# Kernel optimization log

Measured on AMD Instinct MI355X. Metric: run time of the kernel, lower is better.

The kernel has to match this reference:

```python
import jax, jax.numpy as jnp
import numpy as np
import math

B, S, D = 4, 2048, 1024
H, HD = 16, 64
RANK = 16
SCALING = 32.0 / RANK  # alpha / rank = 2.0


def setup_inputs() -> dict:
    key = jax.random.key(0)
    ks = jax.random.split(key, 12)
    s = 1.0 / math.sqrt(D)
    inp = {
        "hidden_states": jax.random.normal(ks[0], (B, S, D), dtype=jnp.float32),
        "attention_mask": jnp.zeros((B, 1, 1, S), dtype=jnp.float32),
        "Wq": jax.random.normal(ks[1], (D, D), dtype=jnp.float32) * s,
        "bq": jnp.zeros((D,), dtype=jnp.float32),
        "Aq": jax.random.normal(ks[2], (RANK, D), dtype=jnp.float32) * s,
        "Bq": jax.random.normal(ks[3], (D, RANK), dtype=jnp.float32) * 0.02,
        "Wk": jax.random.normal(ks[4], (D, D), dtype=jnp.float32) * s,
        "bk": jnp.zeros((D,), dtype=jnp.float32),
        "Wv": jax.random.normal(ks[5], (D, D), dtype=jnp.float32) * s,
        "bv": jnp.zeros((D,), dtype=jnp.float32),
        "Av": jax.random.normal(ks[6], (RANK, D), dtype=jnp.float32) * s,
        "Bv": jax.random.normal(ks[7], (D, RANK), dtype=jnp.float32) * 0.02,
        "Wo": jax.random.normal(ks[8], (D, D), dtype=jnp.float32) * s,
        "bo": jnp.zeros((D,), dtype=jnp.float32),
    }
    return inp


def _lora_linear(x, W, b, A, Bm):
    # F.linear(x, W, b) + (x @ A.T @ B.T) * scaling
    return x @ W.T + b + ((x @ A.T) @ Bm.T) * SCALING


def reference(hidden_states, attention_mask, Wq, bq, Aq, Bq, Wk, bk, Wv, bv, Av, Bv, Wo, bo):
    x = hidden_states
    q = _lora_linear(x, Wq, bq, Aq, Bq)          # [B,S,D]
    k = x @ Wk.T + bk                             # [B,S,D]
    v = _lora_linear(x, Wv, bv, Av, Bv)           # [B,S,D]

    def split_heads(t):
        return t.reshape(B, S, H, HD).transpose(0, 2, 1, 3)  # [B,H,S,HD]

    q, k, v = split_heads(q), split_heads(k), split_heads(v)
    scores = jnp.einsum("bhqd,bhkd->bhqk", q, k) / math.sqrt(HD)  # [B,H,S,S]
    scores = scores + attention_mask
    attn = jax.nn.softmax(scores, axis=-1)
    ctx = jnp.einsum("bhqk,bhkd->bhqd", attn, v)  # [B,H,S,HD]
    ctx = ctx.transpose(0, 2, 1, 3).reshape(B, S, D)
    return ctx @ Wo.T + bo
```

## Files before the change

### kernel.cpp

```cpp
#include <hip/hip_runtime.h>
#include <cstdint>


#define D_DIM 1024
#define S_DIM 2048
#define B_DIM 4
#define H_DIM 16
#define HD_DIM 64
#define M_DIM 8192
#define LOG2E 1.44269504f

typedef __bf16 bf16;
typedef unsigned int u32;
typedef __bf16 bf16x2v __attribute__((ext_vector_type(2)));
typedef __bf16 bf16x4v __attribute__((ext_vector_type(4)));
typedef __bf16 bf16x8 __attribute__((ext_vector_type(8)));
typedef float f32x4 __attribute__((ext_vector_type(4)));

typedef __attribute__((address_space(1))) void* as1p;
typedef __attribute__((address_space(3))) void* as3p;

__device__ __forceinline__ void gll16(const void* g, void* l) {
  __builtin_amdgcn_global_load_lds((as1p)(g), (as3p)(l), 16, 0, 0);
}

__device__ __forceinline__ u32 pack_bf16(float lo, float hi) {
  bf16x2v t;
  t[0] = (bf16)lo;
  t[1] = (bf16)hi;
  return __builtin_bit_cast(u32, t);
}

__global__ void convert_x_kernel(const float* __restrict__ x, bf16* __restrict__ xb) {
  const int i = (blockIdx.x * 256 + threadIdx.x) * 8;
  const float4 a = *(const float4*)(x + i);
  const float4 b = *(const float4*)(x + i + 4);
  bf16x8 o;
  o[0] = (bf16)a.x; o[1] = (bf16)a.y; o[2] = (bf16)a.z; o[3] = (bf16)a.w;
  o[4] = (bf16)b.x; o[5] = (bf16)b.y; o[6] = (bf16)b.z; o[7] = (bf16)b.w;
  *(bf16x8*)(xb + i) = o;
}

__global__ void prep_w_kernel(const float* __restrict__ W, const float* __restrict__ A,
                              const float* __restrict__ Bm, bf16* __restrict__ out,
                              int use_lora) {
  const int i = blockIdx.x * 256 + threadIdx.x;
  const int n = i >> 10, k = i & (D_DIM - 1);
  float w = W[i];
  if (use_lora) {
    float acc = 0.f;
#pragma unroll
    for (int r = 0; r < 16; ++r) acc = fmaf(Bm[n * 16 + r], A[r * D_DIM + k], acc);
    w += 2.0f * acc;
  }
  out[i] = (bf16)w;
}

__global__ __launch_bounds__(256) void gemm_qkv_kernel(
    const bf16* __restrict__ X, const bf16* __restrict__ Wqkv,
    const float* __restrict__ bq, const float* __restrict__ bk,
    const float* __restrict__ bv, bf16* __restrict__ Qo, bf16* __restrict__ Ko,
    bf16* __restrict__ Vo) {
  __shared__ __attribute__((aligned(16))) bf16 As[2][128 * 64];
  __shared__ __attribute__((aligned(16))) bf16 Bs[2][128 * 64];
  const int tid = threadIdx.x;
  const int wave = tid >> 6, lane = tid & 63;
  const int quad = lane >> 4, l16 = lane & 15;
  const int m0 = blockIdx.x * 128, n0 = blockIdx.y * 128;
  const int wm = (wave >> 1) * 64, wn = (wave & 1) * 64;
  const int srow = lane >> 3, sblk = lane & 7;

  const f32x4 zero = {0.f, 0.f, 0.f, 0.f};
  f32x4 acc[4][4];
#pragma unroll
  for (int mi = 0; mi < 4; ++mi)
#pragma unroll
    for (int ni = 0; ni < 4; ++ni) acc[mi][ni] = zero;

  auto stage = [&](int kt) {
    const int buf = kt & 1, kb = kt * 64;
#pragma unroll
    for (int it = 0; it < 4; ++it) {
      const int c = it * 4 + wave;
      const int row = c * 8 + srow;
      const int b = sblk ^ (row & 7);
      gll16(X + (size_t)(m0 + row) * D_DIM + kb + b * 8, &As[buf][c * 512 + lane * 8]);
      gll16(Wqkv + (size_t)(n0 + row) * D_DIM + kb + b * 8, &Bs[buf][c * 512 + lane * 8]);
    }
  };
  stage(0);

  for (int kt = 0; kt < D_DIM / 64; ++kt) {
    __syncthreads();
    if (kt + 1 < D_DIM / 64) stage(kt + 1);
    const bf16* as_ = &As[kt & 1][0];
    const bf16* bs_ = &Bs[kt & 1][0];
#pragma unroll
    for (int ks = 0; ks < 2; ++ks) {
      bf16x8 af[4], bfr[4];
#pragma unroll
      for (int mi = 0; mi < 4; ++mi) {
        const int row = wm + mi * 16 + l16;
        af[mi] = *(const bf16x8*)(as_ + row * 64 + (((ks * 4 + quad) ^ (row & 7)) * 8));
      }
#pragma unroll
      for (int ni = 0; ni < 4; ++ni) {
        const int row = wn + ni * 16 + l16;
        bfr[ni] = *(const bf16x8*)(bs_ + row * 64 + (((ks * 4 + quad) ^ (row & 7)) * 8));
      }
#pragma unroll
      for (int mi = 0; mi < 4; ++mi)
#pragma unroll
        for (int ni = 0; ni < 4; ++ni)
          acc[mi][ni] =
              __builtin_amdgcn_mfma_f32_16x16x32_bf16(af[mi], bfr[ni], acc[mi][ni], 0, 0, 0);
    }
  }

  const int sel = n0 >> 10;
  const float* bp = (sel == 0) ? bq : (sel == 1) ? bk : bv;
  const float qs = 0.125f * LOG2E;

  if (sel == 2) {
#pragma unroll
    for (int ni = 0; ni < 4; ++ni) {
      const int c = (n0 + wn + ni * 16 + l16) & 1023;
      const int h = c >> 6, hd = c & 63;
      const float bvv = bp[c];
#pragma unroll
      for (int mi = 0; mi < 4; ++mi) {
        const int row0 = m0 + wm + mi * 16 + quad * 4;
        const int b = row0 >> 11, s0 = row0 & (S_DIM - 1);
        bf16x4v pk;
#pragma unroll
        for (int r = 0; r < 4; ++r) pk[r] = (bf16)(acc[mi][ni][r] + bvv);
        *(bf16x4v*)(Vo + ((size_t)(b * H_DIM + h) * HD_DIM + hd) * S_DIM + s0) = pk;
      }
    }
  } else {
    bf16* O = (sel == 0) ? Qo : Ko;
#pragma unroll
    for (int ni = 0; ni < 4; ++ni) {
      const int c = (n0 + wn + ni * 16 + l16) & 1023;
      const int h = c >> 6, hd = c & 63;
      const float bvv = bp[c];
#pragma unroll
      for (int mi = 0; mi < 4; ++mi) {
#pragma unroll
        for (int r = 0; r < 4; ++r) {
          const int row = m0 + wm + mi * 16 + quad * 4 + r;
          const int b = row >> 11, s = row & (S_DIM - 1);
          float v = acc[mi][ni][r] + bvv;
          if (sel == 0) v *= qs;
          O[((size_t)(b * H_DIM + h) * S_DIM + s) * HD_DIM + hd] = (bf16)v;
        }
      }
    }
  }
}

__global__ __launch_bounds__(256) void gemm_o_kernel(const bf16* __restrict__ X,
                                                     const bf16* __restrict__ W,
                                                     const float* __restrict__ bias,
                                                     float* __restrict__ out) {
  __shared__ __attribute__((aligned(16))) bf16 As[2][128 * 64];
  __shared__ __attribute__((aligned(16))) bf16 Bs[2][128 * 64];
  const int tid = threadIdx.x;
  const int wave = tid >> 6, lane = tid & 63;
  const int quad = lane >> 4, l16 = lane & 15;
  const int m0 = blockIdx.x * 128, n0 = blockIdx.y * 128;
  const int wm = (wave >> 1) * 64, wn = (wave & 1) * 64;
  const int srow = lane >> 3, sblk = lane & 7;

  const f32x4 zero = {0.f, 0.f, 0.f, 0.f};
  f32x4 acc[4][4];
#pragma unroll
  for (int mi = 0; mi < 4; ++mi)
#pragma unroll
    for (int ni = 0; ni < 4; ++ni) acc[mi][ni] = zero;

  auto stage = [&](int kt) {
    const int buf = kt & 1, kb = kt * 64;
#pragma unroll
    for (int it = 0; it < 4; ++it) {
      const int c = it * 4 + wave;
      const int row = c * 8 + srow;
      const int b = sblk ^ (row & 7);
      gll16(X + (size_t)(m0 + row) * D_DIM + kb + b * 8, &As[buf][c * 512 + lane * 8]);
      gll16(W + (size_t)(n0 + row) * D_DIM + kb + b * 8, &Bs[buf][c * 512 + lane * 8]);
    }
  };
  stage(0);

  for (int kt = 0; kt < D_DIM / 64; ++kt) {
    __syncthreads();
    if (kt + 1 < D_DIM / 64) stage(kt + 1);
    const bf16* as_ = &As[kt & 1][0];
    const bf16* bs_ = &Bs[kt & 1][0];
#pragma unroll
    for (int ks = 0; ks < 2; ++ks) {
      bf16x8 af[4], bfr[4];
#pragma unroll
      for (int mi = 0; mi < 4; ++mi) {
        const int row = wm + mi * 16 + l16;
        af[mi] = *(const bf16x8*)(as_ + row * 64 + (((ks * 4 + quad) ^ (row & 7)) * 8));
      }
#pragma unroll
      for (int ni = 0; ni < 4; ++ni) {
        const int row = wn + ni * 16 + l16;
        bfr[ni] = *(const bf16x8*)(bs_ + row * 64 + (((ks * 4 + quad) ^ (row & 7)) * 8));
      }
#pragma unroll
      for (int mi = 0; mi < 4; ++mi)
#pragma unroll
        for (int ni = 0; ni < 4; ++ni)
          acc[mi][ni] =
              __builtin_amdgcn_mfma_f32_16x16x32_bf16(af[mi], bfr[ni], acc[mi][ni], 0, 0, 0);
    }
  }
#pragma unroll
  for (int ni = 0; ni < 4; ++ni) {
    const int col = n0 + wn + ni * 16 + l16;
    const float bv = bias[col];
#pragma unroll
    for (int mi = 0; mi < 4; ++mi)
#pragma unroll
      for (int r = 0; r < 4; ++r) {
        const int row = m0 + wm + mi * 16 + quad * 4 + r;
        out[(size_t)row * D_DIM + col] = acc[mi][ni][r] + bv;
      }
  }
}

__global__ __launch_bounds__(512, 4) void attn_kernel(const bf16* __restrict__ Q,
                                                      const bf16* __restrict__ K,
                                                      const bf16* __restrict__ Vt,
                                                      const float* __restrict__ mask,
                                                      bf16* __restrict__ ctx) {
  __shared__ __attribute__((aligned(16))) bf16 Ks[2][64 * 64];
  __shared__ __attribute__((aligned(16))) bf16 Vs[2][64 * 64];
  __shared__ __attribute__((aligned(16))) float cms[S_DIM];

  const int tid = threadIdx.x;
  const int wave = tid >> 6, lane = tid & 63;
  const int quad = lane >> 4, l16 = lane & 15;
  const int bh = blockIdx.y, b = bh >> 4, h = bh & 15;
  const int qt = blockIdx.x;

  const bf16* Qg = Q + ((size_t)bh * S_DIM + qt * 256 + wave * 32) * HD_DIM;
  bf16x8 qf[2][2];
#pragma unroll
  for (int nq = 0; nq < 2; ++nq)
#pragma unroll
    for (int ks = 0; ks < 2; ++ks)
      qf[nq][ks] = *(const bf16x8*)(Qg + (nq * 16 + l16) * HD_DIM + ks * 32 + quad * 8);

  {
    const float* mp = mask + b * S_DIM + tid * 4;
    const float4 a = *(const float4*)(mp);
    f32x4 r0 = {fmaf(a.x, LOG2E, -16.f), fmaf(a.y, LOG2E, -16.f),
                fmaf(a.z, LOG2E, -16.f), fmaf(a.w, LOG2E, -16.f)};
    *(f32x4*)(cms + tid * 4) = r0;
  }

  bf16x8 onef;
#pragma unroll
  for (int j = 0; j < 8; ++j) onef[j] = (bf16)1.0f;

  const f32x4 zero = {0.f, 0.f, 0.f, 0.f};
  f32x4 o[2][4], osum[2];
#pragma unroll
  for (int nq = 0; nq < 2; ++nq) {
    osum[nq] = zero;
#pragma unroll
    for (int nh = 0; nh < 4; ++nh) o[nq][nh] = zero;
  }

  const bf16* Kg0 = K + (size_t)bh * S_DIM * HD_DIM;
  const bf16* Vg0 = Vt + (size_t)bh * HD_DIM * S_DIM;

  auto stage = [&](int t) {
    const int buf = t & 1;
    const bf16* Kg = Kg0 + (size_t)t * 64 * HD_DIM;
    const bf16* Vg = Vg0 + t * 64;
    const int c = wave;
    const int row = c * 8 + (lane >> 3);
    const int blk = (lane & 7) ^ (row & 7);
    gll16(Kg + (size_t)row * HD_DIM + blk * 8, &Ks[buf][c * 512 + lane * 8]);
    gll16(Vg + (size_t)row * S_DIM + blk * 8, &Vs[buf][c * 512 + lane * 8]);
  };
  stage(0);

  for (int t = 0; t < S_DIM / 64; ++t) {
    __syncthreads();
    if (t + 1 < S_DIM / 64) stage(t + 1);
    const bf16* ks_ = &Ks[t & 1][0];
    const bf16* vs_ = &Vs[t & 1][0];

#pragma unroll
    for (int half = 0; half < 2; ++half) {
      u32 pk[2][2][2];
#pragma unroll
      for (int mtl = 0; mtl < 2; ++mtl) {
        const int mt = half * 2 + mtl;
        const f32x4 cm = *(const f32x4*)(cms + t * 64 + mt * 16 + quad * 4);
        f32x4 sc[2];
        sc[0] = cm;
        sc[1] = cm;
#pragma unroll
        for (int ks = 0; ks < 2; ++ks) {
          const int row = mt * 16 + l16;
          const bf16x8 kf =
              *(const bf16x8*)(ks_ + row * 64 + (((ks * 4 + quad) ^ (row & 7)) * 8));
#pragma unroll
          for (int nq = 0; nq < 2; ++nq)
            sc[nq] = __builtin_amdgcn_mfma_f32_16x16x32_bf16(kf, qf[nq][ks], sc[nq], 0, 0, 0);
        }
#pragma unroll
        for (int nq = 0; nq < 2; ++nq) {
          const float e0 = __builtin_amdgcn_exp2f(sc[nq][0]);
          const float e1 = __builtin_amdgcn_exp2f(sc[nq][1]);
          const float e2 = __builtin_amdgcn_exp2f(sc[nq][2]);
          const float e3 = __builtin_amdgcn_exp2f(sc[nq][3]);
          pk[nq][mtl][0] = pack_bf16(e0, e1);
          pk[nq][mtl][1] = pack_bf16(e2, e3);
        }
      }

      bf16x8 vf[4];
#pragma unroll
      for (int nh = 0; nh < 4; ++nh) {
        const int vrow = nh * 16 + l16;
        vf[nh] = *(const bf16x8*)(vs_ + vrow * 64 + (((half * 4 + quad) ^ (vrow & 7)) * 8));
      }

#pragma unroll
      for (int nq = 0; nq < 2; ++nq) {
        auto a0 = __builtin_amdgcn_permlane32_swap(pk[nq][0][0], pk[nq][1][0], false, false);
        auto a1 = __builtin_amdgcn_permlane32_swap(pk[nq][0][1], pk[nq][1][1], false, false);
        auto b0 = __builtin_amdgcn_permlane16_swap(a0[0], a0[1], false, false);
        auto b1 = __builtin_amdgcn_permlane16_swap(a1[0], a1[1], false, false);
        union {
          u32 w[4];
          bf16x8 v;
        } pu;
        pu.w[0] = b0[0];
        pu.w[1] = b1[0];
        pu.w[2] = b0[1];
        pu.w[3] = b1[1];
        const bf16x8 pf = pu.v;
#pragma unroll
        for (int nh = 0; nh < 4; ++nh)
          o[nq][nh] = __builtin_amdgcn_mfma_f32_16x16x32_bf16(pf, vf[nh], o[nq][nh], 0, 0, 0);
        osum[nq] = __builtin_amdgcn_mfma_f32_16x16x32_bf16(pf, onef, osum[nq], 0, 0, 0);
      }
    }
  }

#pragma unroll
  for (int nq = 0; nq < 2; ++nq)
#pragma unroll
    for (int r = 0; r < 4; ++r) {
      const float inv = 1.0f / osum[nq][r];
      const int s = qt * 256 + wave * 32 + nq * 16 + quad * 4 + r;
#pragma unroll
      for (int nh = 0; nh < 4; ++nh)
        ctx[((size_t)b * S_DIM + s) * D_DIM + h * 64 + nh * 16 + l16] =
            (bf16)(o[nq][nh][r] * inv);
    }
}

extern "C" void kernel_launch(void* const* d_in, const int* in_sizes, int n_in,
                              void* d_out, int out_size, void* d_ws, size_t ws_size,
                              hipStream_t stream) {
  const float* x    = (const float*)d_in[0];
  const float* mask = (const float*)d_in[1];
  const float* Wq   = (const float*)d_in[2];
  const float* bq   = (const float*)d_in[3];
  const float* Aq   = (const float*)d_in[4];
  const float* Bq   = (const float*)d_in[5];
  const float* Wk   = (const float*)d_in[6];
  const float* bk   = (const float*)d_in[7];
  const float* Wv   = (const float*)d_in[8];
  const float* bv   = (const float*)d_in[9];
  const float* Av   = (const float*)d_in[10];
  const float* Bv   = (const float*)d_in[11];
  const float* Wo   = (const float*)d_in[12];
  const float* bo   = (const float*)d_in[13];
  float* out = (float*)d_out;

  bf16* xb   = (bf16*)d_ws;
  bf16* wqkv = xb + (size_t)M_DIM * D_DIM;
  bf16* wo   = wqkv + (size_t)3 * D_DIM * D_DIM;
  bf16* Qw   = wo + (size_t)D_DIM * D_DIM;
  bf16* Kw   = Qw + (size_t)M_DIM * D_DIM;
  bf16* Vw   = Kw + (size_t)M_DIM * D_DIM;
  bf16* Cw   = xb;

  convert_x_kernel<<<M_DIM * D_DIM / (256 * 8), 256, 0, stream>>>(x, xb);
  prep_w_kernel<<<D_DIM * D_DIM / 256, 256, 0, stream>>>(Wq, Aq, Bq, wqkv, 1);
  prep_w_kernel<<<D_DIM * D_DIM / 256, 256, 0, stream>>>(Wk, nullptr, nullptr,
                                                         wqkv + (size_t)D_DIM * D_DIM, 0);
  prep_w_kernel<<<D_DIM * D_DIM / 256, 256, 0, stream>>>(Wv, Av, Bv,
                                                         wqkv + (size_t)2 * D_DIM * D_DIM, 1);
  prep_w_kernel<<<D_DIM * D_DIM / 256, 256, 0, stream>>>(Wo, nullptr, nullptr, wo, 0);

  gemm_qkv_kernel<<<dim3(M_DIM / 128, 3 * D_DIM / 128), 256, 0, stream>>>(
      xb, wqkv, bq, bk, bv, Qw, Kw, Vw);

  attn_kernel<<<dim3(S_DIM / 256, B_DIM * H_DIM), 512, 0, stream>>>(Qw, Kw, Vw, mask, Cw);

  gemm_o_kernel<<<dim3(M_DIM / 128, D_DIM / 128), 256, 0, stream>>>(Cw, wo, bo, out);
}
```

Baseline: 293.1 us.

## Rewrite QKV GEMM as 256x256 tile with 8-wave ping-pong pipelined schedule

The QKV projection GEMM moves from 128x128 tiles with 4 waves to 256x256 tiles with 8 waves. Each wave now computes a 128x64 sub-tile. The K loop is restructured into a hand-scheduled ping-pong: LDS fragment reads, async global-to-LDS staging of A/B halves, and MFMA bursts are interleaved with explicit barriers, vmcnt waits, and setprio around the MFMA blocks. The aim is more data reuse per tile and overlap of memory traffic with matrix math, at the cost of higher register and LDS use (128 KB shared) and a fragile, hand-tuned synchronisation order.

```diff
diff --git a/kernel.cpp b/kernel.cpp
--- a/kernel.cpp
+++ b/kernel.cpp
@@ -30,6 +30,9 @@
   t[1] = (bf16)hi;
   return __builtin_bit_cast(u32, t);
 }
+
+#define PBAR() __builtin_amdgcn_s_barrier()
+#define VMCNT(n) asm volatile("s_waitcnt vmcnt(" #n ")" ::: "memory")
 
 __global__ void convert_x_kernel(const float* __restrict__ x, bf16* __restrict__ xb) {
   const int i = (blockIdx.x * 256 + threadIdx.x) * 8;
@@ -56,65 +59,140 @@
   out[i] = (bf16)w;
 }
 
-__global__ __launch_bounds__(256) void gemm_qkv_kernel(
+__global__ __launch_bounds__(512, 2) void gemm_qkv_kernel(
     const bf16* __restrict__ X, const bf16* __restrict__ Wqkv,
     const float* __restrict__ bq, const float* __restrict__ bk,
     const float* __restrict__ bv, bf16* __restrict__ Qo, bf16* __restrict__ Ko,
     bf16* __restrict__ Vo) {
-  __shared__ __attribute__((aligned(16))) bf16 As[2][128 * 64];
-  __shared__ __attribute__((aligned(16))) bf16 Bs[2][128 * 64];
+  __shared__ __attribute__((aligned(16))) bf16 As[2][2][128 * 64];
+  __shared__ __attribute__((aligned(16))) bf16 Bs[2][2][128 * 64];
+
   const int tid = threadIdx.x;
   const int wave = tid >> 6, lane = tid & 63;
   const int quad = lane >> 4, l16 = lane & 15;
-  const int m0 = blockIdx.x * 128, n0 = blockIdx.y * 128;
-  const int wm = (wave >> 1) * 64, wn = (wave & 1) * 64;
+  const int wr = wave >> 2, wc = wave & 3;
   const int srow = lane >> 3, sblk = lane & 7;
+  const int m0 = blockIdx.x * 256, n0 = blockIdx.y * 256;
+  const int bh_ = wc >> 1;
 
   const f32x4 zero = {0.f, 0.f, 0.f, 0.f};
-  f32x4 acc[4][4];
-#pragma unroll
-  for (int mi = 0; mi < 4; ++mi)
+  f32x4 acc[8][4];
+#pragma unroll
+  for (int mi = 0; mi < 8; ++mi)
 #pragma unroll
     for (int ni = 0; ni < 4; ++ni) acc[mi][ni] = zero;
 
-  auto stage = [&](int kt) {
-    const int buf = kt & 1, kb = kt * 64;
-#pragma unroll
-    for (int it = 0; it < 4; ++it) {
-      const int c = it * 4 + wave;
+  bf16x8 af[4][2];
+  bf16x8 bf0[2][2], bf1[2][2];
+
+  auto stageA = [&](int slot, int h, int kt) {
+#pragma unroll
+    for (int it = 0; it < 2; ++it) {
+      const int c = wave * 2 + it;
       const int row = c * 8 + srow;
-      const int b = sblk ^ (row & 7);
-      gll16(X + (size_t)(m0 + row) * D_DIM + kb + b * 8, &As[buf][c * 512 + lane * 8]);
-      gll16(Wqkv + (size_t)(n0 + row) * D_DIM + kb + b * 8, &Bs[buf][c * 512 + lane * 8]);
+      const int blk = sblk ^ (row & 7);
+      gll16(X + (size_t)(m0 + h * 128 + row) * D_DIM + kt * 64 + blk * 8,
+            &As[slot][h][c * 512 + lane * 8]);
     }
   };
-  stage(0);
-
-  for (int kt = 0; kt < D_DIM / 64; ++kt) {
-    __syncthreads();
-    if (kt + 1 < D_DIM / 64) stage(kt + 1);
-    const bf16* as_ = &As[kt & 1][0];
-    const bf16* bs_ = &Bs[kt & 1][0];
-#pragma unroll
-    for (int ks = 0; ks < 2; ++ks) {
-      bf16x8 af[4], bfr[4];
-#pragma unroll
-      for (int mi = 0; mi < 4; ++mi) {
-        const int row = wm + mi * 16 + l16;
-        af[mi] = *(const bf16x8*)(as_ + row * 64 + (((ks * 4 + quad) ^ (row & 7)) * 8));
-      }
-#pragma unroll
-      for (int ni = 0; ni < 4; ++ni) {
-        const int row = wn + ni * 16 + l16;
-        bfr[ni] = *(const bf16x8*)(bs_ + row * 64 + (((ks * 4 + quad) ^ (row & 7)) * 8));
-      }
-#pragma unroll
-      for (int mi = 0; mi < 4; ++mi)
-#pragma unroll
-        for (int ni = 0; ni < 4; ++ni)
-          acc[mi][ni] =
-              __builtin_amdgcn_mfma_f32_16x16x32_bf16(af[mi], bfr[ni], acc[mi][ni], 0, 0, 0);
-    }
+  auto stageB = [&](int slot, int h, int kt) {
+#pragma unroll
+    for (int it = 0; it < 2; ++it) {
+      const int c = wave * 2 + it;
+      const int row = c * 8 + srow;
+      const int blk = sblk ^ (row & 7);
+      gll16(Wqkv + (size_t)(n0 + h * 128 + row) * D_DIM + kt * 64 + blk * 8,
+            &Bs[slot][h][c * 512 + lane * 8]);
+    }
+  };
+
+#define LDSA(AB, MH)                                                           \
+  _Pragma("unroll") for (int mi2 = 0; mi2 < 4; ++mi2)                          \
+      _Pragma("unroll") for (int ks = 0; ks < 2; ++ks) {                       \
+    const int lr = (MH)*64 + mi2 * 16 + l16;                                   \
+    af[mi2][ks] =                                                              \
+        *(const bf16x8*)((AB) + lr * 64 + (((ks * 4 + quad) ^ (lr & 7)) * 8)); \
+  }
+#define LDSB(BB, NH, BF)                                                       \
+  _Pragma("unroll") for (int ni2 = 0; ni2 < 2; ++ni2)                          \
+      _Pragma("unroll") for (int ks = 0; ks < 2; ++ks) {                       \
+    const int lr = (wc & 1) * 64 + ((NH)*2 + ni2) * 16 + l16;                  \
+    BF[ni2][ks] =                                                              \
+        *(const bf16x8*)((BB) + lr * 64 + (((ks * 4 + quad) ^ (lr & 7)) * 8)); \
+  }
+#define MMA8(MH, NH, BF)                                                       \
+  __builtin_amdgcn_s_setprio(1);                                               \
+  _Pragma("unroll") for (int mi2 = 0; mi2 < 4; ++mi2)                          \
+      _Pragma("unroll") for (int ni2 = 0; ni2 < 2; ++ni2)                      \
+          _Pragma("unroll") for (int ks = 0; ks < 2; ++ks) {                   \
+    acc[(MH)*4 + mi2][(NH)*2 + ni2] = __builtin_amdgcn_mfma_f32_16x16x32_bf16( \
+        af[mi2][ks], BF[ni2][ks], acc[(MH)*4 + mi2][(NH)*2 + ni2], 0, 0, 0);   \
+  }                                                                            \
+  __builtin_amdgcn_s_setprio(0);
+
+  const bf16* a0p = &As[0][wr][0];
+  const bf16* a1p = &As[1][wr][0];
+  const bf16* b0p = &Bs[0][bh_][0];
+  const bf16* b1p = &Bs[1][bh_][0];
+
+  stageB(0, 0, 0);
+  stageB(0, 1, 0);
+  stageA(0, 0, 0);
+  stageA(0, 1, 0);
+  stageB(1, 0, 1);
+  stageB(1, 1, 1);
+  VMCNT(4);
+  PBAR();
+
+  for (int j = 0; j < 8; ++j) {
+    const bool more = (j < 7);
+    const int ktA1 = 2 * j + 1, ktN0 = 2 * j + 2, ktN1 = 2 * j + 3;
+    LDSA(a0p, 0);
+    LDSB(b0p, 0, bf0);
+    stageA(1, 0, ktA1);
+    PBAR();
+    MMA8(0, 0, bf0);
+    PBAR();
+    LDSB(b0p, 1, bf1);
+    stageA(1, 1, ktA1);
+    PBAR();
+    MMA8(0, 1, bf1);
+    PBAR();
+    LDSA(a0p, 1);
+    if (more) stageB(0, 0, ktN0);
+    PBAR();
+    MMA8(1, 1, bf1);
+    PBAR();
+    if (more) stageB(0, 1, ktN0);
+    PBAR();
+    MMA8(1, 0, bf0);
+    if (more) {
+      VMCNT(4);
+    } else {
+      VMCNT(0);
+    }
+    PBAR();
+    LDSA(a1p, 0);
+    LDSB(b1p, 0, bf0);
+    if (more) stageA(0, 0, ktN0);
+    PBAR();
+    MMA8(0, 0, bf0);
+    PBAR();
+    LDSB(b1p, 1, bf1);
+    if (more) stageA(0, 1, ktN0);
+    PBAR();
+    MMA8(0, 1, bf1);
+    PBAR();
+    LDSA(a1p, 1);
+    if (more) stageB(1, 0, ktN1);
+    PBAR();
+    MMA8(1, 1, bf1);
+    PBAR();
+    if (more) stageB(1, 1, ktN1);
+    PBAR();
+    MMA8(1, 0, bf0);
+    VMCNT(4);
+    PBAR();
   }
 
   const int sel = n0 >> 10;
@@ -124,12 +202,12 @@
   if (sel == 2) {
 #pragma unroll
     for (int ni = 0; ni < 4; ++ni) {
-      const int c = (n0 + wn + ni * 16 + l16) & 1023;
+      const int c = (n0 + wc * 64 + ni * 16 + l16) & 1023;
       const int h = c >> 6, hd = c & 63;
       const float bvv = bp[c];
 #pragma unroll
-      for (int mi = 0; mi < 4; ++mi) {
-        const int row0 = m0 + wm + mi * 16 + quad * 4;
+      for (int mi = 0; mi < 8; ++mi) {
+        const int row0 = m0 + wr * 128 + mi * 16 + quad * 4;
         const int b = row0 >> 11, s0 = row0 & (S_DIM - 1);
         bf16x4v pk;
 #pragma unroll
@@ -141,14 +219,14 @@
     bf16* O = (sel == 0) ? Qo : Ko;
 #pragma unroll
     for (int ni = 0; ni < 4; ++ni) {
-      const int c = (n0 + wn + ni * 16 + l16) & 1023;
+      const int c = (n0 + wc * 64 + ni * 16 + l16) & 1023;
       const int h = c >> 6, hd = c & 63;
       const float bvv = bp[c];
 #pragma unroll
-      for (int mi = 0; mi < 4; ++mi) {
+      for (int mi = 0; mi < 8; ++mi) {
 #pragma unroll
         for (int r = 0; r < 4; ++r) {
-          const int row = m0 + wm + mi * 16 + quad * 4 + r;
+          const int row = m0 + wr * 128 + mi * 16 + quad * 4 + r;
           const int b = row >> 11, s = row & (S_DIM - 1);
           float v = acc[mi][ni][r] + bvv;
           if (sel == 0) v *= qs;
@@ -157,6 +235,9 @@
       }
     }
   }
+#undef LDSA
+#undef LDSB
+#undef MMA8
 }
 
 __global__ __launch_bounds__(256) void gemm_o_kernel(const bf16* __restrict__ X,
@@ -405,7 +486,7 @@
                                                          wqkv + (size_t)2 * D_DIM * D_DIM, 1);
   prep_w_kernel<<<D_DIM * D_DIM / 256, 256, 0, stream>>>(Wo, nullptr, nullptr, wo, 0);
 
-  gemm_qkv_kernel<<<dim3(M_DIM / 128, 3 * D_DIM / 128), 256, 0, stream>>>(
+  gemm_qkv_kernel<<<dim3(M_DIM / 256, 3 * D_DIM / 256), 512, 0, stream>>>(
       xb, wqkv, bq, bk, bv, Qw, Kw, Vw);
 
   attn_kernel<<<dim3(S_DIM / 256, B_DIM * H_DIM), 512, 0, stream>>>(Qw, Kw, Vw, mask, Cw);
```

Measured after the change: 311.8 us. 6.4% more time.
